# Kernel tuning notes

Measured on AMD Instinct MI355X. Metric: run time of the kernel, lower is better.

The kernel has to match this reference:

```python
import jax, jax.numpy as jnp
import numpy as np

B, D, H, O, RH, P = 8192, 784, 2048, 1024, 128, 64
NI = NJ = NK = 4  # input regions / hidden groups / output groups


def _make_groups():
    idx = np.arange(28 * 28).reshape(28, 28)
    input_groups = np.stack([
        idx[:14, :14].ravel(), idx[:14, 14:].ravel(),
        idx[14:, :14].ravel(), idx[14:, 14:].ravel(),
    ]).astype(np.int32)                                   # [4, 196]
    hidden_groups = np.arange(H, dtype=np.int32).reshape(NJ, H // NJ)   # [4, 512]
    output_groups = np.arange(O, dtype=np.int32).reshape(NK, O // NK)   # [4, 256]
    return input_groups, hidden_groups, output_groups


def setup_inputs() -> dict:
    key = jax.random.key(0)
    ks = jax.random.split(key, 9)
    ig, hg, og = _make_groups()
    inp = {
        "x":   jax.random.normal(ks[0], (B, D), jnp.float32),
        "W1":  jax.random.normal(ks[1], (H, D), jnp.float32) / np.sqrt(D),
        "b1":  jax.random.normal(ks[2], (H,), jnp.float32) * 0.01,
        "W2":  jax.random.normal(ks[3], (O, H), jnp.float32) / np.sqrt(H),
        "b2":  jax.random.normal(ks[4], (O,), jnp.float32) * 0.01,
        "Wr1": jax.random.normal(ks[5], (RH, D), jnp.float32) / np.sqrt(D),
        "br1": jax.random.normal(ks[6], (RH,), jnp.float32) * 0.01,
        "Wr2": jax.random.normal(ks[7], (P, RH), jnp.float32) / np.sqrt(RH),
        "br2": jax.random.normal(ks[8], (P,), jnp.float32) * 0.01,
        "input_groups": jnp.asarray(ig),
        "hidden_groups": jnp.asarray(hg),
        "output_groups": jnp.asarray(og),
        "top_k": 8,
    }
    return inp


def reference(x, W1, b1, W2, b2, Wr1, br1, Wr2, br2,
              input_groups, hidden_groups, output_groups, top_k):
    # --- router MLP (eval mode: dropout = identity, no routing noise) ---
    h_r = jax.nn.relu(x @ Wr1.T + br1)
    scores = h_r @ Wr2.T + br2                      # [B, P]
    probs = jax.nn.softmax(scores, axis=-1)         # temperature = 1.0

    # --- top-k pathway selection + renormalization ---
    top_vals, top_idx = jax.lax.top_k(probs, top_k)
    bsz = x.shape[0]
    mask = jnp.zeros_like(probs).at[jnp.arange(bsz)[:, None], top_idx].set(top_vals)
    wts = mask / (mask.sum(axis=-1, keepdims=True) + 1e-8)
    wts4 = wts.reshape(bsz, NI, NJ, NK)             # pathway_idx = i*16 + j*4 + k

    # --- gather pathway sub-blocks ---
    x_reg = x[:, input_groups]                      # [B, I, 196]
    # W1g[i, j] = W1[hidden_groups[j]][:, input_groups[i]] -> [I, J, 512, 196]
    W1g = W1[hidden_groups[None, :, :, None], input_groups[:, None, None, :]]
    b1g = b1[hidden_groups]                         # [J, 512]
    # W2g[j, k] = W2[output_groups[k]][:, hidden_groups[j]] -> [J, K, 256, 512]
    W2g = W2[output_groups[None, :, :, None], hidden_groups[:, None, None, :]]
    b2g = b2[output_groups]                         # [K, 256]

    # --- pathway computation (exact erf GELU, as torch F.gelu default) ---
    hidden = jax.nn.gelu(
        jnp.einsum('bin,ijhn->ijbh', x_reg, W1g) + b1g[None, :, None, :],
        approximate=False)                          # [I, J, B, 512]
    # weighted pathway outputs, contracted over i, j, h without materializing
    # the full [I, J, K, B, 256] tensor
    out_main = jnp.einsum('ijbh,jkoh,bijk->bko', hidden, W2g, wts4)  # [B, K, 256]
    wsum = wts4.sum(axis=(1, 2))                    # [B, K] (bias weighted per pathway)
    out_blocks = out_main + wsum[:, :, None] * b2g[None]

    out = jnp.zeros((bsz, O), x.dtype).at[:, output_groups].add(out_blocks)
    return out
```

## Files before the change

### kernel.cpp

```cpp
#include <hip/hip_runtime.h>
#include <hip/hip_bf16.h>
#include <hip/hip_fp16.h>

#define B_  8192
#define D_  784
#define H_  2048
#define O_  1024
#define RH_ 128
#define P_  64
#define KP  224
#define KR  800

typedef __attribute__((ext_vector_type(8))) short short8;
typedef __attribute__((ext_vector_type(8))) _Float16 h16x8;
typedef __attribute__((ext_vector_type(4))) float f32x4;

__device__ inline float bf2f(unsigned short u) {
  union { unsigned int i; float f; } v; v.i = ((unsigned int)u) << 16; return v.f;
}
__device__ inline unsigned short f2bf(float f) {
  __hip_bfloat16 h = __float2bfloat16(f);
  return *reinterpret_cast<unsigned short*>(&h);
}
__device__ inline unsigned short f2h(float f) {
  __half h = __float2half(f);
  return *reinterpret_cast<unsigned short*>(&h);
}
__device__ inline float h2f(unsigned short u) {
  __half h = *reinterpret_cast<__half*>(&u);
  return __half2float(h);
}
__device__ inline float erf_fast(float x) {
  float ax = fabsf(x);
  float t = 1.0f / (1.0f + 0.3275911f * ax);
  float p = ((((1.061405429f * t - 1.453152027f) * t + 1.421413741f) * t
              - 0.284496736f) * t + 0.254829592f) * t;
  float y = 1.0f - p * __expf(-ax * ax);
  return x < 0.f ? -y : y;
}
__device__ inline float gelu_exact(float v) {
  return 0.5f * v * (1.0f + erf_fast(v * 0.70710678118654752f));
}

__device__ inline void gload_lds16(const void* g, void* l) {
  __builtin_amdgcn_global_load_lds((const __attribute__((address_space(1))) void*)g,
                                   (__attribute__((address_space(3))) void*)l, 16, 0, 0);
}

template <bool F16>
__device__ inline void gemm128_db(const unsigned short* gA0, const unsigned short* gA1,
                                  const unsigned short* gB0, const unsigned short* gB1,
                                  int K, char* lds, f32x4 acc[4][4]) {
  const int t = threadIdx.x;
  const int w = t >> 6, l = t & 63;
  const int wr = (w >> 1) * 64, wc = (w & 1) * 64;
  const int lr = l & 15;
  const int swr = (lr >> 1) & 3;
  const int arow = (wr + lr) * 64 + (((l >> 4) ^ swr) * 16);
  const int brow = 8192 + (wc + lr) * 64 + (((l >> 4) ^ swr) * 16);
  const int tOff = t * 16;
  {
    char* d = lds + tOff;
    gload_lds16(gA0, d);
    gload_lds16(gA1, d + 4096);
    gload_lds16(gB0, d + 8192);
    gload_lds16(gB1, d + 12288);
  }
  int cur = 0;
  for (int kt = 0; kt < K; kt += 32) {
    const int nxt = kt + 32;
    if (nxt < K) {
      char* d = lds + ((cur ^ 1) << 14) + tOff;
      gload_lds16(gA0 + nxt, d);
      gload_lds16(gA1 + nxt, d + 4096);
      gload_lds16(gB0 + nxt, d + 8192);
      gload_lds16(gB1 + nxt, d + 12288);
      __builtin_amdgcn_sched_barrier(0);
      asm volatile("s_waitcnt vmcnt(4)" ::: "memory");
    } else {
      __builtin_amdgcn_sched_barrier(0);
      asm volatile("s_waitcnt vmcnt(0)" ::: "memory");
    }
    __builtin_amdgcn_sched_barrier(0);
    __builtin_amdgcn_s_barrier();
    __builtin_amdgcn_sched_barrier(0);
    const char* buf = lds + (cur << 14);
    short8 af[4], bfr[4];
#pragma unroll
    for (int f = 0; f < 4; ++f) {
      af[f]  = *(const short8*)(buf + arow + f * 1024);
      bfr[f] = *(const short8*)(buf + brow + f * 1024);
    }
#pragma unroll
    for (int fm = 0; fm < 4; ++fm)
#pragma unroll
      for (int fn = 0; fn < 4; ++fn) {
        if constexpr (F16)
          acc[fm][fn] = __builtin_amdgcn_mfma_f32_16x16x32_f16(
              (h16x8)af[fm], (h16x8)bfr[fn], acc[fm][fn], 0, 0, 0);
        else
          acc[fm][fn] = __builtin_amdgcn_mfma_f32_16x16x32_bf16(af[fm], bfr[fn], acc[fm][fn], 0, 0, 0);
      }
    __builtin_amdgcn_sched_barrier(0);
    __builtin_amdgcn_s_barrier();
    __builtin_amdgcn_sched_barrier(0);
    cur ^= 1;
  }
}

__device__ inline void gemm128_db64(const unsigned short* gA0, const unsigned short* gA1,
                                    const unsigned short* gB0, const unsigned short* gB1,
                                    int K, char* lds, f32x4 acc[4][4]) {
  const int t = threadIdx.x;
  const int w = t >> 6, l = t & 63;
  const int wr = (w >> 1) * 64, wc = (w & 1) * 64;
  const int lr = l & 15;
  const int swr = (lr >> 1) & 3;
  const int arow = (wr + lr) * 64 + (((l >> 4) ^ swr) * 16);
  const int brow = 8192 + (wc + lr) * 64 + (((l >> 4) ^ swr) * 16);
  const int tOff = t * 16;
#define STAGE64(bufbase, ksrc) { \
    char* d = lds + (bufbase) + tOff; \
    gload_lds16(gA0 + (ksrc), d); \
    gload_lds16(gA1 + (ksrc), d + 4096); \
    gload_lds16(gB0 + (ksrc), d + 8192); \
    gload_lds16(gB1 + (ksrc), d + 12288); \
    gload_lds16(gA0 + (ksrc) + 32, d + 16384); \
    gload_lds16(gA1 + (ksrc) + 32, d + 16384 + 4096); \
    gload_lds16(gB0 + (ksrc) + 32, d + 16384 + 8192); \
    gload_lds16(gB1 + (ksrc) + 32, d + 16384 + 12288); \
  }
  STAGE64(0, 0);
  int cur = 0;
  for (int kt = 0; kt < K; kt += 64) {
    if (kt + 64 < K) {
      STAGE64((cur ^ 1) << 15, kt + 64);
      __builtin_amdgcn_sched_barrier(0);
      asm volatile("s_waitcnt vmcnt(8)" ::: "memory");
    } else {
      __builtin_amdgcn_sched_barrier(0);
      asm volatile("s_waitcnt vmcnt(0)" ::: "memory");
    }
    __builtin_amdgcn_sched_barrier(0);
    __builtin_amdgcn_s_barrier();
    __builtin_amdgcn_sched_barrier(0);
    const char* buf = lds + (cur << 15);
#pragma unroll
    for (int c = 0; c < 2; ++c) {
      const char* ch = buf + c * 16384;
      short8 af[4], bfr[4];
#pragma unroll
      for (int f = 0; f < 4; ++f) {
        af[f]  = *(const short8*)(ch + arow + f * 1024);
        bfr[f] = *(const short8*)(ch + brow + f * 1024);
      }
#pragma unroll
      for (int fm = 0; fm < 4; ++fm)
#pragma unroll
        for (int fn = 0; fn < 4; ++fn)
          acc[fm][fn] = __builtin_amdgcn_mfma_f32_16x16x32_bf16(af[fm], bfr[fn], acc[fm][fn], 0, 0, 0);
    }
    __builtin_amdgcn_sched_barrier(0);
    __builtin_amdgcn_s_barrier();
    __builtin_amdgcn_sched_barrier(0);
    cur ^= 1;
  }
#undef STAGE64
}

__device__ inline void gemm128_bt64(const unsigned short* __restrict__ A,
                                    const unsigned short* __restrict__ Bm,
                                    int K, char* lds, f32x4 acc[4][4]) {
  const int t = threadIdx.x;
  const int s_orig = (t & 3) ^ ((t >> 3) & 3);
  const size_t srcOff = (size_t)(t >> 2) * K + s_orig * 8;
  gemm128_db64(A + srcOff, A + srcOff + (size_t)64 * K,
               Bm + srcOff, Bm + srcOff + (size_t)64 * K, K, lds, acc);
}

__global__ void k_prep(const float* __restrict__ x, const float* __restrict__ W1,
                       const float* __restrict__ W2, const int* __restrict__ ig,
                       const float* __restrict__ Wr1,
                       unsigned short* __restrict__ xreg, unsigned short* __restrict__ w1g,
                       unsigned short* __restrict__ w2b,
                       unsigned short* __restrict__ xsp, unsigned short* __restrict__ wr1sp) {
  const size_t N1 = (size_t)4 * B_ * KP;
  const size_t N2 = (size_t)4 * H_ * KP;
  const size_t N3 = (size_t)O_ * H_;
  const size_t N4 = (size_t)B_ * KR;
  const size_t N5 = (size_t)RH_ * KR;
  const size_t TOT = N1 + N2 + N3 + N4 + N5;
  for (size_t idx = (size_t)blockIdx.x * blockDim.x + threadIdx.x; idx < TOT;
       idx += (size_t)gridDim.x * blockDim.x) {
    if (idx < N1) {
      int n = (int)(idx % KP); size_t r = idx / KP;
      int b = (int)(r % B_); int i = (int)(r / B_);
      float v = (n < 196) ? x[(size_t)b * D_ + ig[i * 196 + n]] : 0.f;
      xreg[idx] = f2bf(v);
    } else if (idx < N1 + N2) {
      size_t q = idx - N1;
      int n = (int)(q % KP); size_t r = q / KP;
      int h = (int)(r % H_); int i = (int)(r / H_);
      float v = (n < 196) ? W1[(size_t)h * D_ + ig[i * 196 + n]] : 0.f;
      w1g[q] = f2bf(v);
    } else if (idx < N1 + N2 + N3) {
      size_t q = idx - N1 - N2;
      w2b[q] = f2bf(W2[q]);
    } else if (idx < N1 + N2 + N3 + N4) {
      size_t q = idx - N1 - N2 - N3;
      int c = (int)(q % KR); int b = (int)(q / KR);
      float v = (c < D_) ? x[(size_t)b * D_ + c] : 0.f;
      unsigned short hi = f2h(v);
      unsigned short lo = f2h(v - h2f(hi));
      xsp[(size_t)b * (2 * KR) + c]      = hi;
      xsp[(size_t)b * (2 * KR) + KR + c] = lo;
    } else {
      size_t q = idx - N1 - N2 - N3 - N4;
      int c = (int)(q % KR); int h = (int)(q / KR);
      float v = (c < D_) ? Wr1[(size_t)h * D_ + c] : 0.f;
      unsigned short hi = f2h(v);
      unsigned short lo = f2h(v - h2f(hi));
      wr1sp[(size_t)h * KR + c]                    = hi;
      wr1sp[(size_t)RH_ * KR + h * KR + c]         = hi;
      wr1sp[(size_t)2 * RH_ * KR + h * KR + c]     = lo;
    }
  }
}

__global__ __launch_bounds__(256) void k_r1m(const unsigned short* __restrict__ xsp,
    const unsigned short* __restrict__ wr1sp, float* __restrict__ hrp) {
  __shared__ __align__(128) char lds[32768];
  const int mt = blockIdx.x, z = blockIdx.y;
  const int t = threadIdx.x;
  const int aoff = (z == 1) ? KR : 0;
  const int s_orig = (t & 3) ^ ((t >> 3) & 3);
  const int scol = s_orig * 8;
  const unsigned short* gA0 = xsp + ((size_t)(mt * 128) + (t >> 2)) * (2 * KR) + aoff + scol;
  const unsigned short* gA1 = gA0 + (size_t)64 * (2 * KR);
  const unsigned short* gB0 = wr1sp + (size_t)z * RH_ * KR + (size_t)(t >> 2) * KR + scol;
  const unsigned short* gB1 = gB0 + (size_t)64 * KR;
  f32x4 acc[4][4];
#pragma unroll
  for (int a = 0; a < 4; ++a)
#pragma unroll
    for (int b = 0; b < 4; ++b) acc[a][b] = (f32x4){0.f, 0.f, 0.f, 0.f};
  gemm128_db<true>(gA0, gA1, gB0, gB1, KR, lds, acc);
  float* hz = hrp + (size_t)z * B_ * RH_;
  const int w = t >> 6, l = t & 63;
  const int rbase = mt * 128 + (w >> 1) * 64 + (l >> 4) * 4;
  const int cb = (w & 1) * 64 + (l & 15);
#pragma unroll
  for (int fn = 0; fn < 4; ++fn) {
    const int h = cb + fn * 16;
#pragma unroll
    for (int fm = 0; fm < 4; ++fm)
#pragma unroll
      for (int r = 0; r < 4; ++r)
        hz[(size_t)(rbase + fm * 16 + r) * RH_ + h] = acc[fm][fn][r];
  }
}

#define R2S 32
__global__ __launch_bounds__(256) void k_r2(const float* __restrict__ hrp,
    const float* __restrict__ br1,
    const float* __restrict__ Wr2, const float* __restrict__ br2,
    float* __restrict__ wts, float* __restrict__ wsum,
    unsigned long long* __restrict__ actmask) {
  __shared__ float Ws[64][130];
  __shared__ float hs[R2S][128];
  const int s0 = blockIdx.x * R2S;
  const int t = threadIdx.x;
  for (int idx = t; idx < 2048; idx += 256) {
    int r = idx >> 5, c = (idx & 31) * 4;
    *(float4*)&Ws[r][c] = *(const float4*)(Wr2 + (size_t)r * RH_ + c);
  }
  for (int idx = t; idx < R2S * 32; idx += 256) {
    int r = idx >> 5, c = (idx & 31) * 4;
    const size_t off = (size_t)(s0 + r) * RH_ + c;
    float4 p0 = *(const float4*)(hrp + off);
    float4 p1 = *(const float4*)(hrp + (size_t)1 * B_ * RH_ + off);
    float4 p2 = *(const float4*)(hrp + (size_t)2 * B_ * RH_ + off);
    float4 bb = *(const float4*)(br1 + c);
    float4 s;
    s.x = fmaxf(p0.x + p1.x + p2.x + bb.x, 0.f);
    s.y = fmaxf(p0.y + p1.y + p2.y + bb.y, 0.f);
    s.z = fmaxf(p0.z + p1.z + p2.z + bb.z, 0.f);
    s.w = fmaxf(p0.w + p1.w + p2.w + bb.w, 0.f);
    *(float4*)&hs[r][c] = s;
  }
  __syncthreads();
  const int w = t >> 6, p = t & 63;
  const float wb2 = br2[p];
  for (int si = 0; si < R2S / 4; ++si) {
    const int sl = w * (R2S / 4) + si;
    float sc = wb2;
#pragma unroll
    for (int kk = 0; kk < 32; ++kk) {
      float4 h4 = *(const float4*)&hs[sl][kk * 4];
      float4 w4 = *(const float4*)&Ws[p][kk * 4];
      sc += h4.x * w4.x + h4.y * w4.y + h4.z * w4.z + h4.w * w4.w;
    }
    float m = sc;
#pragma unroll
    for (int o = 32; o; o >>= 1) m = fmaxf(m, __shfl_xor(m, o));
    float e = __expf(sc - m);
    float Z = e;
#pragma unroll
    for (int o = 32; o; o >>= 1) Z += __shfl_xor(Z, o);
    bool sel = false;
    float ssum = 0.f;
    for (int it = 0; it < 8; ++it) {
      float v = sel ? -1.f : e;
      float vm = v;
#pragma unroll
      for (int o = 32; o; o >>= 1) vm = fmaxf(vm, __shfl_xor(vm, o));
      unsigned long long mask = __ballot(!sel && v == vm);
      int first = __ffsll((long long)mask) - 1;
      if (p == first) sel = true;
      ssum += vm;
    }
    const float dn = 1.0f / (ssum + 1e-8f * Z);
    const float wv = sel ? e * dn : 0.f;
    wts[(size_t)(s0 + sl) * 64 + p] = wv;
    const unsigned long long am = __ballot(sel);
    if (p == 0) actmask[s0 + sl] = am;
    float part = wv;
#pragma unroll
    for (int o = 4; o < 64; o <<= 1) part += __shfl_xor(part, o);
    if (p < 4) wsum[(size_t)(s0 + sl) * 4 + p] = part;
  }
}

__global__ __launch_bounds__(256) void k_compact(const unsigned long long* __restrict__ actmask,
                                                 int* __restrict__ lists,
                                                 int* __restrict__ counts) {
  __shared__ int wcnt[4];
  __shared__ int sbase;
  const int ij = blockIdx.x;
  const int shift = (ij >> 2) * 16 + (ij & 3) * 4;
  const int t = threadIdx.x;
  const int wid = t >> 6, lane = t & 63;
  unsigned long long mk[32];
#pragma unroll
  for (int c = 0; c < 32; ++c) mk[c] = actmask[c * 256 + t];
  if (t == 0) sbase = 0;
  __syncthreads();
  for (int c = 0; c < 32; ++c) {
    const int b = c * 256 + t;
    const bool act = ((mk[c] >> shift) & 0xFULL) != 0ULL;
    const unsigned long long m = __ballot(act);
    if (lane == 0) wcnt[wid] = __popcll(m);
    __syncthreads();
    int off = sbase;
    const int tot = wcnt[0] + wcnt[1] + wcnt[2] + wcnt[3];
    for (int q = 0; q < wid; ++q) off += wcnt[q];
    if (act)
      lists[ij * B_ + off + __popcll(m & ((1ULL << lane) - 1ULL))] = b;
    __syncthreads();
    if (t == 0) sbase += tot;
  }
  __syncthreads();
  if (t == 0) counts[ij] = sbase;
}

__global__ __launch_bounds__(256) void k_l1g(const unsigned short* __restrict__ xreg,
    const unsigned short* __restrict__ w1g, const float* __restrict__ b1,
    const int* __restrict__ lists, const int* __restrict__ counts,
    unsigned short* __restrict__ hid16) {
  const int mt = blockIdx.x, nt = blockIdx.y, iq = blockIdx.z;
  const int ij = iq * 4 + (nt >> 2);
  const int count = counts[ij];
  if (mt * 128 >= count) return;
  __shared__ __align__(128) char lds[32768];
  __shared__ int rows[128];
  const int t = threadIdx.x;
  const int* list = lists + (size_t)ij * B_;
  if (t < 128) {
    int rl = mt * 128 + t;
    rows[t] = list[rl < count ? rl : count - 1];
  }
  __syncthreads();
  const int s_orig = (t & 3) ^ ((t >> 3) & 3);
  const int scol = s_orig * 8;
  const int r0 = rows[t >> 2], r1 = rows[(t >> 2) + 64];
  const unsigned short* gA0 = xreg + ((size_t)iq * B_ + r0) * KP + scol;
  const unsigned short* gA1 = xreg + ((size_t)iq * B_ + r1) * KP + scol;
  const unsigned short* gB0 = w1g + ((size_t)(iq * H_ + nt * 128) + (t >> 2)) * KP + scol;
  const unsigned short* gB1 = gB0 + (size_t)64 * KP;
  f32x4 acc[4][4];
#pragma unroll
  for (int a = 0; a < 4; ++a)
#pragma unroll
    for (int b = 0; b < 4; ++b) acc[a][b] = (f32x4){0.f, 0.f, 0.f, 0.f};
  gemm128_db<false>(gA0, gA1, gB0, gB1, KP, lds, acc);
  const int w = t >> 6, l = t & 63;
  const int rloc0 = (w >> 1) * 64 + (l >> 4) * 4;
  const int cloc = (w & 1) * 64 + (l & 15);
  unsigned short* lt = (unsigned short*)lds;
  __syncthreads();
#pragma unroll
  for (int fn = 0; fn < 4; ++fn) {
    const int col = cloc + fn * 16;
    const float bias = b1[nt * 128 + col];
#pragma unroll
    for (int fm = 0; fm < 4; ++fm)
#pragma unroll
      for (int r = 0; r < 4; ++r) {
        const int row = rloc0 + fm * 16 + r;
        const int gsw = (col >> 3) ^ (row & 7);
        lt[row * 128 + gsw * 8 + (col & 7)] = f2h(acc[fm][fn][r] + bias);
      }
  }
  __syncthreads();
  const int mlim = count - mt * 128;
  const int row = t >> 1, half = t & 1;
  if (row < mlim) {
    unsigned short* dst = hid16 + ((size_t)iq * B_ + rows[row]) * H_ + nt * 128 + half * 64;
#pragma unroll
    for (int q = 0; q < 8; ++q) {
      const int g = (half * 8 + q) ^ (row & 7);
      *(short8*)(dst + q * 8) = *(const short8*)(lt + row * 128 + g * 8);
    }
  }
}

__global__ __launch_bounds__(256) void k_combine(unsigned short* __restrict__ hid,
                                                 const float* __restrict__ wts) {
  const int b = blockIdx.x;
  const int n = threadIdx.x * 8;
  const int j = n >> 9;
  const float* wb = wts + (size_t)b * 64 + j * 4;
  float acc[4][8];
#pragma unroll
  for (int k = 0; k < 4; ++k)
#pragma unroll
    for (int e = 0; e < 8; ++e) acc[k][e] = 0.f;
#pragma unroll
  for (int i = 0; i < 4; ++i) {
    const float4 w4 = *(const float4*)(wb + i * 16);
    if (w4.x != 0.f || w4.y != 0.f || w4.z != 0.f || w4.w != 0.f) {
      short8 raw = *(const short8*)(hid + ((size_t)i * B_ + b) * H_ + n);
#pragma unroll
      for (int e = 0; e < 8; ++e) {
        float g = gelu_exact(h2f((unsigned short)raw[e]));
        acc[0][e] += g * w4.x;
        acc[1][e] += g * w4.y;
        acc[2][e] += g * w4.z;
        acc[3][e] += g * w4.w;
      }
    }
  }
#pragma unroll
  for (int k = 0; k < 4; ++k) {
    short8 outv;
#pragma unroll
    for (int e = 0; e < 8; ++e) outv[e] = (short)f2bf(acc[k][e]);
    *(short8*)(hid + ((size_t)k * B_ + b) * H_ + n) = outv;
  }
}

__global__ __launch_bounds__(256) void k_l2(const unsigned short* __restrict__ G,
    const unsigned short* __restrict__ w2b, const float* __restrict__ b2,
    const float* __restrict__ wsum, float* __restrict__ out) {
  __shared__ __align__(128) char lds[65536];
  const int mt = blockIdx.x, nt = blockIdx.y, k = blockIdx.z;
  const unsigned short* A  = G + ((size_t)k * B_ + mt * 128) * H_;
  const unsigned short* Bm = w2b + ((size_t)(k * 256 + nt * 128)) * H_;
  f32x4 acc[4][4];
#pragma unroll
  for (int a = 0; a < 4; ++a)
#pragma unroll
    for (int b = 0; b < 4; ++b) acc[a][b] = (f32x4){0.f, 0.f, 0.f, 0.f};
  gemm128_bt64(A, Bm, H_, lds, acc);
  const int t = threadIdx.x, w = t >> 6, l = t & 63;
  const int rbase = mt * 128 + (w >> 1) * 64 + (l >> 4) * 4;
  const int cb = nt * 128 + (w & 1) * 64 + (l & 15);
#pragma unroll
  for (int fn = 0; fn < 4; ++fn) {
    const int ncol = k * 256 + cb + fn * 16;
    const float bias = b2[ncol];
#pragma unroll
    for (int fm = 0; fm < 4; ++fm)
#pragma unroll
      for (int r = 0; r < 4; ++r) {
        const int m = rbase + fm * 16 + r;
        out[(size_t)m * O_ + ncol] = acc[fm][fn][r] + wsum[m * 4 + k] * bias;
      }
  }
}

extern "C" void kernel_launch(void* const* d_in, const int* in_sizes, int n_in,
                              void* d_out, int out_size, void* d_ws, size_t ws_size,
                              hipStream_t stream) {
  const float* x   = (const float*)d_in[0];
  const float* W1  = (const float*)d_in[1];
  const float* b1  = (const float*)d_in[2];
  const float* W2  = (const float*)d_in[3];
  const float* b2  = (const float*)d_in[4];
  const float* Wr1 = (const float*)d_in[5];
  const float* br1 = (const float*)d_in[6];
  const float* Wr2 = (const float*)d_in[7];
  const float* br2 = (const float*)d_in[8];
  const int*   ig  = (const int*)d_in[9];
  float* out = (float*)d_out;
  char* ws = (char*)d_ws;
  unsigned short* xreg = (unsigned short*)(ws);
  unsigned short* w1g  = (unsigned short*)(ws + 14680064);
  unsigned short* w2b  = (unsigned short*)(ws + 18350080);
  float*          wts  = (float*)(ws + 22544384);
  float*          wsum = (float*)(ws + 24641536);
  unsigned short* hid  = (unsigned short*)(ws + 24772608);
  float*          hrp   = (float*)(ws + 24772608);
  unsigned short* xsp   = (unsigned short*)(ws + 24772608 + 12582912);
  unsigned short* wr1sp = (unsigned short*)(ws + 24772608 + 38797312);
  int*                lists   = (int*)d_out;
  int*                counts  = lists + 16 * B_;
  unsigned long long* actmask = (unsigned long long*)((char*)d_out + 524352);

  k_prep<<<dim3(2048), dim3(256), 0, stream>>>(x, W1, W2, ig, Wr1, xreg, w1g, w2b, xsp, wr1sp);
  k_r1m<<<dim3(B_ / 128, 3), dim3(256), 0, stream>>>(xsp, wr1sp, hrp);
  k_r2<<<dim3(B_ / R2S), dim3(256), 0, stream>>>(hrp, br1, Wr2, br2, wts, wsum, actmask);
  k_compact<<<dim3(16), dim3(256), 0, stream>>>(actmask, lists, counts);
  k_l1g<<<dim3(B_ / 128, H_ / 128, 4), dim3(256), 0, stream>>>(xreg, w1g, b1, lists, counts, hid);
  k_combine<<<dim3(B_), dim3(256), 0, stream>>>(hid, wts);
  k_l2<<<dim3(B_ / 128, 2, 4), dim3(256), 0, stream>>>(hid, w2b, b2, wsum, out);
}
```

Before: 207.1 us.

## Keep gathered A tile resident in LDS and loop over four N tiles per block

The layer-1 gathered GEMM now loads the full 128-row x K tile of routed activations into LDS once. Each block then loops over the four 128-column hidden tiles of its group, streaming only the W1 tiles through a double buffer. This cuts repeated gathers of the same activation rows across N tiles and reduces block count and launch overhead. In exchange it uses 72KB of LDS with a launch bound of 2 blocks per CU and serializes four tiles per block. The epilogue is split into two 64-row halves to fit the staging buffer.

```diff
diff --git a/kernel.cpp b/kernel.cpp
--- a/kernel.cpp
+++ b/kernel.cpp
@@ -363,15 +363,16 @@
   if (t == 0) counts[ij] = sbase;
 }
 
-__global__ __launch_bounds__(256) void k_l1g(const unsigned short* __restrict__ xreg,
+__global__ __launch_bounds__(256, 2) void k_l1h(const unsigned short* __restrict__ xreg,
     const unsigned short* __restrict__ w1g, const float* __restrict__ b1,
     const int* __restrict__ lists, const int* __restrict__ counts,
     unsigned short* __restrict__ hid16) {
-  const int mt = blockIdx.x, nt = blockIdx.y, iq = blockIdx.z;
-  const int ij = iq * 4 + (nt >> 2);
+  const int ij = blockIdx.y;
+  const int iq = ij >> 2, j = ij & 3;
   const int count = counts[ij];
+  const int mt = blockIdx.x;
   if (mt * 128 >= count) return;
-  __shared__ __align__(128) char lds[32768];
+  __shared__ __align__(128) char lds[73728];
   __shared__ int rows[128];
   const int t = threadIdx.x;
   const int* list = lists + (size_t)ij * B_;
@@ -380,47 +381,106 @@
     rows[t] = list[rl < count ? rl : count - 1];
   }
   __syncthreads();
+  const int w = t >> 6, l = t & 63;
+  const int wc = (w & 1) * 64;
+  const int lr = l & 15;
+  const int swr = (lr >> 1) & 3;
+  const int arow = (((w >> 1) * 64) + lr) * 64 + (((l >> 4) ^ swr) * 16);
+  const int brow = (wc + lr) * 64 + (((l >> 4) ^ swr) * 16);
+  const int tOff = t * 16;
   const int s_orig = (t & 3) ^ ((t >> 3) & 3);
   const int scol = s_orig * 8;
   const int r0 = rows[t >> 2], r1 = rows[(t >> 2) + 64];
   const unsigned short* gA0 = xreg + ((size_t)iq * B_ + r0) * KP + scol;
   const unsigned short* gA1 = xreg + ((size_t)iq * B_ + r1) * KP + scol;
-  const unsigned short* gB0 = w1g + ((size_t)(iq * H_ + nt * 128) + (t >> 2)) * KP + scol;
-  const unsigned short* gB1 = gB0 + (size_t)64 * KP;
-  f32x4 acc[4][4];
-#pragma unroll
-  for (int a = 0; a < 4; ++a)
-#pragma unroll
-    for (int b = 0; b < 4; ++b) acc[a][b] = (f32x4){0.f, 0.f, 0.f, 0.f};
-  gemm128_db<false>(gA0, gA1, gB0, gB1, KP, lds, acc);
-  const int w = t >> 6, l = t & 63;
-  const int rloc0 = (w >> 1) * 64 + (l >> 4) * 4;
-  const int cloc = (w & 1) * 64 + (l & 15);
-  unsigned short* lt = (unsigned short*)lds;
-  __syncthreads();
-#pragma unroll
-  for (int fn = 0; fn < 4; ++fn) {
-    const int col = cloc + fn * 16;
-    const float bias = b1[nt * 128 + col];
-#pragma unroll
-    for (int fm = 0; fm < 4; ++fm)
-#pragma unroll
-      for (int r = 0; r < 4; ++r) {
-        const int row = rloc0 + fm * 16 + r;
-        const int gsw = (col >> 3) ^ (row & 7);
-        lt[row * 128 + gsw * 8 + (col & 7)] = f2h(acc[fm][fn][r] + bias);
-      }
-  }
-  __syncthreads();
+  char* ldsA = lds;
+  char* ldsB = lds + 57344;
+#pragma unroll
+  for (int ks = 0; ks < 7; ++ks) {
+    gload_lds16(gA0 + ks * 32, ldsA + ks * 8192 + tOff);
+    gload_lds16(gA1 + ks * 32, ldsA + ks * 8192 + 4096 + tOff);
+  }
   const int mlim = count - mt * 128;
-  const int row = t >> 1, half = t & 1;
-  if (row < mlim) {
-    unsigned short* dst = hid16 + ((size_t)iq * B_ + rows[row]) * H_ + nt * 128 + half * 64;
-#pragma unroll
-    for (int q = 0; q < 8; ++q) {
-      const int g = (half * 8 + q) ^ (row & 7);
-      *(short8*)(dst + q * 8) = *(const short8*)(lt + row * 128 + g * 8);
-    }
+  for (int ntl = 0; ntl < 4; ++ntl) {
+    const int nt = j * 4 + ntl;
+    const unsigned short* gB0 = w1g + ((size_t)(iq * H_ + nt * 128) + (t >> 2)) * KP + scol;
+    const unsigned short* gB1 = gB0 + (size_t)64 * KP;
+    gload_lds16(gB0, ldsB + tOff);
+    gload_lds16(gB1, ldsB + 4096 + tOff);
+    f32x4 acc[4][4];
+#pragma unroll
+    for (int a = 0; a < 4; ++a)
+#pragma unroll
+      for (int b = 0; b < 4; ++b) acc[a][b] = (f32x4){0.f, 0.f, 0.f, 0.f};
+    int cur = 0;
+#pragma unroll
+    for (int ks = 0; ks < 7; ++ks) {
+      if (ks < 6) {
+        char* d = ldsB + ((cur ^ 1) << 13) + tOff;
+        gload_lds16(gB0 + (ks + 1) * 32, d);
+        gload_lds16(gB1 + (ks + 1) * 32, d + 4096);
+        __builtin_amdgcn_sched_barrier(0);
+        asm volatile("s_waitcnt vmcnt(2)" ::: "memory");
+      } else {
+        __builtin_amdgcn_sched_barrier(0);
+        asm volatile("s_waitcnt vmcnt(0)" ::: "memory");
+      }
+      __builtin_amdgcn_sched_barrier(0);
+      __builtin_amdgcn_s_barrier();
+      __builtin_amdgcn_sched_barrier(0);
+      const char* bufA = ldsA + ks * 8192;
+      const char* bufB = ldsB + (cur << 13);
+      short8 af[4], bfr[4];
+#pragma unroll
+      for (int f = 0; f < 4; ++f) {
+        af[f]  = *(const short8*)(bufA + arow + f * 1024);
+        bfr[f] = *(const short8*)(bufB + brow + f * 1024);
+      }
+#pragma unroll
+      for (int fm = 0; fm < 4; ++fm)
+#pragma unroll
+        for (int fn = 0; fn < 4; ++fn)
+          acc[fm][fn] = __builtin_amdgcn_mfma_f32_16x16x32_bf16(af[fm], bfr[fn], acc[fm][fn], 0, 0, 0);
+      __builtin_amdgcn_sched_barrier(0);
+      __builtin_amdgcn_s_barrier();
+      __builtin_amdgcn_sched_barrier(0);
+      cur ^= 1;
+    }
+    const float bias0 = b1[nt * 128 + wc + lr];
+    const float bias1 = b1[nt * 128 + wc + 16 + lr];
+    const float bias2 = b1[nt * 128 + wc + 32 + lr];
+    const float bias3 = b1[nt * 128 + wc + 48 + lr];
+    unsigned short* lt = (unsigned short*)ldsB;
+    for (int rr = 0; rr < 2; ++rr) {
+      __syncthreads();
+      if ((w >> 1) == rr) {
+#pragma unroll
+        for (int fm = 0; fm < 4; ++fm)
+#pragma unroll
+          for (int r = 0; r < 4; ++r) {
+            const int rir = (l >> 4) * 4 + fm * 16 + r;
+#pragma unroll
+            for (int fn = 0; fn < 4; ++fn) {
+              const int col = wc + fn * 16 + lr;
+              const int gsw = (col >> 3) ^ (rir & 7);
+              const float bias = (fn == 0) ? bias0 : (fn == 1) ? bias1 : (fn == 2) ? bias2 : bias3;
+              lt[rir * 128 + gsw * 8 + (col & 7)] = f2h(acc[fm][fn][r] + bias);
+            }
+          }
+      }
+      __syncthreads();
+      const int rir = t >> 2;
+      const int rowglob = rr * 64 + rir;
+      if (rowglob < mlim) {
+        unsigned short* dst = hid16 + ((size_t)iq * B_ + rows[rowglob]) * H_ + nt * 128;
+#pragma unroll
+        for (int q = 0; q < 4; ++q) {
+          const int g = (t & 3) * 4 + q;
+          *(short8*)(dst + g * 8) = *(const short8*)(lt + rir * 128 + (g ^ (rir & 7)) * 8);
+        }
+      }
+    }
+    __syncthreads();
   }
 }
 
@@ -521,7 +581,7 @@
   k_r1m<<<dim3(B_ / 128, 3), dim3(256), 0, stream>>>(xsp, wr1sp, hrp);
   k_r2<<<dim3(B_ / R2S), dim3(256), 0, stream>>>(hrp, br1, Wr2, br2, wts, wsum, actmask);
   k_compact<<<dim3(16), dim3(256), 0, stream>>>(actmask, lists, counts);
-  k_l1g<<<dim3(B_ / 128, H_ / 128, 4), dim3(256), 0, stream>>>(xreg, w1g, b1, lists, counts, hid);
+  k_l1h<<<dim3(64, 16), dim3(256), 0, stream>>>(xreg, w1g, b1, lists, counts, hid);
   k_combine<<<dim3(B_), dim3(256), 0, stream>>>(hid, wts);
   k_l2<<<dim3(B_ / 128, 2, 4), dim3(256), 0, stream>>>(hid, w2b, b2, wsum, out);
 }
```

Measured after the change: 212.7 us. +2.7%, slower.
